# Kernel tuning notes

Measured on AMD Instinct MI355X. Metric: run time of the kernel, lower is better.

## Reference

```python
import jax, jax.numpy as jnp
import numpy as np

D_MODEL = 1024
NUM_HEAD = 16
HEAD_DIM = D_MODEL // NUM_HEAD
S, B = 2048, 2


def setup_inputs() -> dict:
    key = jax.random.key(0)
    ks = jax.random.split(key, 8)
    q = jax.random.normal(ks[0], (S, B, D_MODEL), dtype=jnp.float32)
    k = jax.random.normal(ks[1], (S, B, D_MODEL), dtype=jnp.float32)
    v = jax.random.normal(ks[2], (S, B, D_MODEL), dtype=jnp.float32)
    attn_mask = jnp.zeros((S, S), dtype=jnp.float32)
    # xavier_uniform_ bound for square (D,D) linear: sqrt(6/(D+D))
    bound = float(np.sqrt(6.0 / (D_MODEL + D_MODEL)))
    def w(k_):
        return jax.random.uniform(k_, (D_MODEL, D_MODEL), jnp.float32, -bound, bound)
    Wq, Wk, Wv, Wo = w(ks[3]), w(ks[4]), w(ks[5]), w(ks[6])
    zb = jnp.zeros((D_MODEL,), jnp.float32)
    return {"q": q, "k": k, "v": v, "attn_mask": attn_mask,
            "Wq": Wq, "bq": zb, "Wk": Wk, "bk": zb,
            "Wv": Wv, "bv": zb, "Wo": Wo, "bo": zb}


def reference(q, k, v, attn_mask, Wq, bq, Wk, bk, Wv, bv, Wo, bo):
    s, b, d = q.shape
    h, hd = NUM_HEAD, HEAD_DIM
    # QKV projections (torch Linear: x @ W.T + b)
    qp = q @ Wq.T + bq  # (S,B,D)
    kp = k @ Wk.T + bk
    vp = v @ Wv.T + bv
    # (S,B,H,Dh) -> permute(2,1,0,3) -> (H,B,S,Dh)
    qh = jnp.transpose(qp.reshape(s, b, h, hd), (2, 1, 0, 3))
    kh = jnp.transpose(kp.reshape(s, b, h, hd), (2, 1, 0, 3))
    vh = jnp.transpose(vp.reshape(s, b, h, hd), (2, 1, 0, 3))
    scores = jnp.einsum('hbqd,hbkd->hbqk', qh, kh) / jnp.sqrt(jnp.float32(hd))
    scores = scores + attn_mask  # additive mask broadcast over (H,B,*,*)
    weights = jax.nn.softmax(scores, axis=-1)
    out = jnp.einsum('hbqk,hbkd->hbqd', weights, vh)  # (H,B,S,Dh)
    # Faithful to original: raw contiguous view (H,B,S,Dh) -> (S,B,D)
    out = out.reshape(s, b, d)
    return out @ Wo.T + bo
```

## Files before the change

kernel.cpp:

```cpp
#include <hip/hip_runtime.h>
#include <hip/hip_bf16.h>
#include <cstdint>
#include <cstddef>

typedef unsigned short u16;
typedef short bf16x8 __attribute__((ext_vector_type(8)));
typedef short bf16x4 __attribute__((ext_vector_type(4)));
typedef unsigned short u16x8 __attribute__((ext_vector_type(8)));
typedef unsigned short u16x4 __attribute__((ext_vector_type(4)));
typedef float f32x4 __attribute__((ext_vector_type(4)));

#define S_LEN 2048
#define BATCH 2
#define DM 1024
#define NHEAD 16
#define HDIM 64
#define MROWS (S_LEN * BATCH)
#define LOG2E 1.44269504088896340736f
#define KSPLIT 2
#define SPAN (S_LEN / KSPLIT)
#define NROWS (NHEAD * BATCH * S_LEN)

__device__ __forceinline__ u16 f32_to_bf16(float f) {
  union { float f; uint32_t u; } v; v.f = f;
  uint32_t u = v.u;
  u += 0x7FFFu + ((u >> 16) & 1u);
  return (u16)(u >> 16);
}
__device__ __forceinline__ u16 cvt_bf16(float f) {
  __hip_bfloat16 h = __float2bfloat16(f);
  return *reinterpret_cast<u16*>(&h);
}
__device__ __forceinline__ float bf2f(u16 x) {
  union { float f; uint32_t u; } v; v.u = ((uint32_t)x) << 16; return v.f;
}

__device__ __forceinline__ void gload_lds16(const void* g, void* l) {
  __builtin_amdgcn_global_load_lds(
      (const __attribute__((address_space(1))) void*)g,
      (__attribute__((address_space(3))) void*)l, 16, 0, 0);
}

__device__ __forceinline__ bf16x4 tr_read(const void* lp) {
  bf16x4 d;
  auto p = (const __attribute__((address_space(3))) short*)lp;
  asm volatile("ds_read_b64_tr_b16 %0, %1" : "=v"(d) : "v"(p));
  return d;
}

#if __has_builtin(__builtin_amdgcn_mfma_f32_16x16x16_bf16)
#define MFMA16(a, b, c) __builtin_amdgcn_mfma_f32_16x16x16_bf16(a, b, c, 0, 0, 0)
#elif __has_builtin(__builtin_amdgcn_mfma_f32_16x16x16bf16_1k)
#define MFMA16(a, b, c) __builtin_amdgcn_mfma_f32_16x16x16bf16_1k(a, b, c, 0, 0, 0)
#else
__device__ __forceinline__ f32x4 mfma16_asm(bf16x4 a, bf16x4 b, f32x4 c) {
  f32x4 d;
  asm volatile("v_mfma_f32_16x16x16_bf16 %0, %1, %2, %3\n\ts_nop 7\n\ts_nop 7"
               : "=&v"(d) : "v"(a), "v"(b), "v"(c));
  return d;
}
#define MFMA16(a, b, c) mfma16_asm(a, b, c)
#endif

__global__ void cast4_f32_bf16(const float* __restrict__ s0, u16* __restrict__ d0,
                               const float* __restrict__ s1, u16* __restrict__ d1,
                               const float* __restrict__ s2, u16* __restrict__ d2,
                               const float* __restrict__ s3, u16* __restrict__ d3,
                               float4 scales, int n8) {
  const int which = blockIdx.y;
  const float* src = which == 0 ? s0 : which == 1 ? s1 : which == 2 ? s2 : s3;
  u16* dst = which == 0 ? d0 : which == 1 ? d1 : which == 2 ? d2 : d3;
  const float sc = which == 0 ? scales.x : which == 1 ? scales.y : which == 2 ? scales.z : scales.w;
  int i = blockIdx.x * blockDim.x + threadIdx.x;
  const int stride = gridDim.x * blockDim.x;
  for (; i < n8; i += stride) {
    const float4* s = (const float4*)(src + (size_t)i * 8);
    float4 a = s[0];
    float4 b = s[1];
    u16x8 o;
    o[0] = f32_to_bf16(a.x * sc); o[1] = f32_to_bf16(a.y * sc);
    o[2] = f32_to_bf16(a.z * sc); o[3] = f32_to_bf16(a.w * sc);
    o[4] = f32_to_bf16(b.x * sc); o[5] = f32_to_bf16(b.y * sc);
    o[6] = f32_to_bf16(b.z * sc); o[7] = f32_to_bf16(b.w * sc);
    *(u16x8*)(dst + (size_t)i * 8) = o;
  }
}

template <int MODE>
__global__ __launch_bounds__(256) void gemm_bt(
    const u16* __restrict__ A, const u16* __restrict__ Bw, const float* __restrict__ bias,
    float* __restrict__ outF, u16* __restrict__ outP, int M, int N, int K, float oscale)
{
  __shared__ u16 As[128 * 32];
  __shared__ u16 Bs[64 * 32];
  const int tid = threadIdx.x;
  const int wave = tid >> 6, lane = tid & 63;
  const int l15 = lane & 15, l4 = lane >> 4;
  const int wr = wave >> 1, wc = wave & 1;
  const int rowBase = blockIdx.y * 128, colBase = blockIdx.x * 64;

  f32x4 acc[4][2];
#pragma unroll
  for (int m = 0; m < 4; ++m)
#pragma unroll
    for (int n = 0; n < 2; ++n) acc[m][n] = (f32x4){0.f, 0.f, 0.f, 0.f};

  for (int k0 = 0; k0 < K; k0 += 32) {
#pragma unroll
    for (int c = 0; c < 2; ++c) {
      const int ldsbyte = wave * 2048 + c * 1024;
      const int elt = (ldsbyte >> 1) + lane * 8;
      const int r = elt >> 5, cc = elt & 31;
      gload_lds16(A + (size_t)(rowBase + r) * K + k0 + cc, (char*)As + ldsbyte);
    }
    {
      const int ldsbyte = wave * 1024;
      const int elt = (ldsbyte >> 1) + lane * 8;
      const int r = elt >> 5, cc = elt & 31;
      gload_lds16(Bw + (size_t)(colBase + r) * K + k0 + cc, (char*)Bs + ldsbyte);
    }
    __syncthreads();

    bf16x8 af[4], bfr[2];
#pragma unroll
    for (int m = 0; m < 4; ++m)
      af[m] = *(const bf16x8*)&As[(wr * 64 + m * 16 + l15) * 32 + 8 * l4];
#pragma unroll
    for (int n = 0; n < 2; ++n)
      bfr[n] = *(const bf16x8*)&Bs[(wc * 32 + n * 16 + l15) * 32 + 8 * l4];
#pragma unroll
    for (int m = 0; m < 4; ++m)
#pragma unroll
      for (int n = 0; n < 2; ++n)
        acc[m][n] = __builtin_amdgcn_mfma_f32_16x16x32_bf16(af[m], bfr[n], acc[m][n], 0, 0, 0);
    __syncthreads();
  }

#pragma unroll
  for (int m = 0; m < 4; ++m)
#pragma unroll
    for (int n = 0; n < 2; ++n)
#pragma unroll
      for (int j = 0; j < 4; ++j) {
        const int row = rowBase + wr * 64 + m * 16 + 4 * l4 + j;
        const int col = colBase + wc * 32 + n * 16 + l15;
        const float vv = (acc[m][n][j] + bias[col]) * oscale;
        if (MODE == 0) {
          const int s = row >> 1, b = row & 1, h = col >> 6, dh = col & 63;
          outP[((size_t)(h * BATCH + b) * S_LEN + s) * HDIM + dh] = f32_to_bf16(vv);
        } else {
          outF[(size_t)row * N + col] = vv;
        }
      }
}

__device__ __forceinline__ void stageK_swz(const u16* __restrict__ Kp, int kt, u16* dst, int tid) {
#pragma unroll
  for (int h = 0; h < 2; ++h) {
    const int c = tid + 256 * h;
    const int r = c >> 3, x = c & 7;
    gload_lds16(Kp + (size_t)(kt + r) * HDIM + (x ^ (r & 7)) * 8, (char*)dst + 16 * c);
  }
}
__device__ __forceinline__ void stageV(const u16* __restrict__ Vp, int kt, u16* dst, int tid) {
#pragma unroll
  for (int h = 0; h < 2; ++h) {
    const int c = tid + 256 * h;
    const int key = 4 * ((c >> 3) & 15) + ((c >> 1) & 3);
    const int dh  = 16 * (c >> 7) + 8 * (c & 1);
    gload_lds16(Vp + (size_t)(kt + key) * HDIM + dh, (char*)dst + 16 * c);
  }
}

__global__ __launch_bounds__(256, 4) void flash_attn(
    const u16* __restrict__ Qh, const u16* __restrict__ Kh, const u16* __restrict__ Vh,
    const u16* __restrict__ maskb, u16* __restrict__ Opart, float2* __restrict__ mlp)
{
  const int hb = blockIdx.y;
  const int z  = blockIdx.z;
  const int qb = blockIdx.x * 128;
  const int kbase = z * SPAN;
  const u16* Qp = Qh + (size_t)hb * S_LEN * HDIM;
  const u16* Kp = Kh + (size_t)hb * S_LEN * HDIM + (size_t)kbase * HDIM;
  const u16* Vp = Vh + (size_t)hb * S_LEN * HDIM + (size_t)kbase * HDIM;
  const u16* mp = maskb + kbase;
  const int tid = threadIdx.x;
  const int wave = tid >> 6, lane = tid & 63;
  const int l15 = lane & 15, l4 = lane >> 4;
  const int qrow0 = qb + wave * 32 + l15;
  const int qrow1 = qrow0 + 16;

  __shared__ u16 Klds[2][4096];
  __shared__ u16 Vlds[2][4096];

  bf16x8 bq[2][2];
  bq[0][0] = *(const bf16x8*)&Qp[(size_t)qrow0 * HDIM + 8 * l4];
  bq[0][1] = *(const bf16x8*)&Qp[(size_t)qrow0 * HDIM + 32 + 8 * l4];
  bq[1][0] = *(const bf16x8*)&Qp[(size_t)qrow1 * HDIM + 8 * l4];
  bq[1][1] = *(const bf16x8*)&Qp[(size_t)qrow1 * HDIM + 32 + 8 * l4];

  stageK_swz(Kp, 0, &Klds[0][0], tid);
  stageV(Vp, 0, &Vlds[0][0], tid);

  float m_run[2] = {-1e30f, -1e30f}, l_run[2] = {0.f, 0.f};
  f32x4 oacc[2][4];
#pragma unroll
  for (int f = 0; f < 2; ++f)
#pragma unroll
    for (int D = 0; D < 4; ++D) oacc[f][D] = (f32x4){0.f, 0.f, 0.f, 0.f};

  __syncthreads();

  for (int kt = 0; kt < SPAN; kt += 64) {
    const int cur = (kt >> 6) & 1;
    if (kt + 64 < SPAN) {
      stageK_swz(Kp, kt + 64, &Klds[cur ^ 1][0], tid);
      stageV(Vp, kt + 64, &Vlds[cur ^ 1][0], tid);
    }
    u16x4 mc[2][4];
#pragma unroll
    for (int kb = 0; kb < 4; ++kb) {
      mc[0][kb] = *(const u16x4*)&mp[(size_t)qrow0 * S_LEN + kt + 16 * kb + 4 * l4];
      mc[1][kb] = *(const u16x4*)&mp[(size_t)qrow1 * S_LEN + kt + 16 * kb + 4 * l4];
    }

    bf16x4 pb[2][4];
#pragma unroll
    for (int f = 0; f < 2; ++f) {
      f32x4 st[4];
#pragma unroll
      for (int kb = 0; kb < 4; ++kb) {
        const int r = 16 * kb + l15;
        const int s0 = (l4 ^ (l15 & 7)) * 8;
        const int s1 = ((l4 + 4) ^ (l15 & 7)) * 8;
        bf16x8 k0 = *(const bf16x8*)&Klds[cur][r * 64 + s0];
        bf16x8 k1 = *(const bf16x8*)&Klds[cur][r * 64 + s1];
        f32x4 zz = (f32x4){0.f, 0.f, 0.f, 0.f};
        zz = __builtin_amdgcn_mfma_f32_16x16x32_bf16(k0, bq[f][0], zz, 0, 0, 0);
        zz = __builtin_amdgcn_mfma_f32_16x16x32_bf16(k1, bq[f][1], zz, 0, 0, 0);
        st[kb] = zz;
      }
      float p[16];
#pragma unroll
      for (int kb = 0; kb < 4; ++kb)
#pragma unroll
        for (int j = 0; j < 4; ++j)
          p[4 * kb + j] = st[kb][j] + bf2f((u16)mc[f][kb][j]);

      float t0 = fmaxf(fmaxf(p[0], p[1]), fmaxf(p[2], p[3]));
      float t1 = fmaxf(fmaxf(p[4], p[5]), fmaxf(p[6], p[7]));
      float t2 = fmaxf(fmaxf(p[8], p[9]), fmaxf(p[10], p[11]));
      float t3 = fmaxf(fmaxf(p[12], p[13]), fmaxf(p[14], p[15]));
      float tm = fmaxf(fmaxf(t0, t1), fmaxf(t2, t3));
      tm = fmaxf(tm, __shfl_xor(tm, 16));
      tm = fmaxf(tm, __shfl_xor(tm, 32));

      if (!__all(tm - m_run[f] <= 11.0f)) {
        const float mn_ = fmaxf(m_run[f], tm);
        const float fac = exp2f(m_run[f] - mn_);
#pragma unroll
        for (int D = 0; D < 4; ++D)
#pragma unroll
          for (int j = 0; j < 4; ++j) oacc[f][D][j] *= fac;
        l_run[f] *= fac;
        m_run[f] = mn_;
      }

      float rs = 0.f;
#pragma unroll
      for (int kb = 0; kb < 4; ++kb)
#pragma unroll
        for (int e = 0; e < 4; ++e) {
          const float pe = exp2f(p[4 * kb + e] - m_run[f]);
          rs += pe;
          pb[f][kb][e] = (short)cvt_bf16(pe);
        }
      rs += __shfl_xor(rs, 16);
      rs += __shfl_xor(rs, 32);
      l_run[f] += rs;
    }

    const char* vb = (const char*)&Vlds[cur][0] + 8 * lane;
#pragma unroll
    for (int g = 0; g < 2; ++g) {
      bf16x4 va[2][4];
#pragma unroll
      for (int D = 0; D < 2; ++D)
#pragma unroll
        for (int kb = 0; kb < 4; ++kb)
          va[D][kb] = tr_read(vb + 2048 * (2 * g + D) + 512 * kb);
      asm volatile("s_waitcnt lgkmcnt(0)" ::: "memory");
      __builtin_amdgcn_sched_barrier(0);
#pragma unroll
      for (int D = 0; D < 2; ++D)
#pragma unroll
        for (int kb = 0; kb < 4; ++kb) {
          oacc[0][2 * g + D] = MFMA16(va[D][kb], pb[0][kb], oacc[0][2 * g + D]);
          oacc[1][2 * g + D] = MFMA16(va[D][kb], pb[1][kb], oacc[1][2 * g + D]);
        }
    }

    __syncthreads();
  }

  u16* Oz = Opart + (size_t)z * NROWS * HDIM;
#pragma unroll
  for (int f = 0; f < 2; ++f) {
    const float inv = 1.0f / l_run[f];
    const int qr = f == 0 ? qrow0 : qrow1;
    const size_t row = (size_t)hb * S_LEN + qr;
#pragma unroll
    for (int D = 0; D < 4; ++D) {
      u16x4 ov;
#pragma unroll
      for (int j = 0; j < 4; ++j) ov[j] = f32_to_bf16(oacc[f][D][j] * inv);
      *(u16x4*)&Oz[row * HDIM + 16 * D + 4 * l4] = ov;
    }
    if (l4 == 0) mlp[(size_t)z * NROWS + row] = make_float2(m_run[f], l_run[f]);
  }
}

__global__ __launch_bounds__(256) void fa_combine(
    const u16* __restrict__ Opart, const float2* __restrict__ mlp, u16* __restrict__ Ob)
{
  const int idx = blockIdx.x * blockDim.x + threadIdx.x;
  const int row = idx >> 4, c = idx & 15;
  const float2 a = mlp[row];
  const float2 b = mlp[NROWS + row];
  const float m = fmaxf(a.x, b.x);
  float w0 = exp2f(a.x - m) * a.y;
  float w1 = exp2f(b.x - m) * b.y;
  const float inv = 1.f / (w0 + w1);
  w0 *= inv; w1 *= inv;
  const size_t off = (size_t)row * HDIM + 4 * c;
  const u16x4 o0 = *(const u16x4*)&Opart[off];
  const u16x4 o1 = *(const u16x4*)&Opart[(size_t)NROWS * HDIM + off];
  u16x4 o;
#pragma unroll
  for (int j = 0; j < 4; ++j)
    o[j] = f32_to_bf16(w0 * bf2f((u16)o0[j]) + w1 * bf2f((u16)o1[j]));
  *(u16x4*)&Ob[off] = o;
}

extern "C" void kernel_launch(void* const* d_in, const int* in_sizes, int n_in,
                              void* d_out, int out_size, void* d_ws, size_t ws_size,
                              hipStream_t stream) {
  const float* q    = (const float*)d_in[0];
  const float* k    = (const float*)d_in[1];
  const float* v    = (const float*)d_in[2];
  const float* mask = (const float*)d_in[3];
  const float* Wq   = (const float*)d_in[4];
  const float* bq   = (const float*)d_in[5];
  const float* Wk   = (const float*)d_in[6];
  const float* bk   = (const float*)d_in[7];
  const float* Wv   = (const float*)d_in[8];
  const float* bv   = (const float*)d_in[9];
  const float* Wo   = (const float*)d_in[10];
  const float* bo   = (const float*)d_in[11];
  float* out = (float*)d_out;

  char* ws = (char*)d_ws;
  const size_t TEN = (size_t)MROWS * DM * sizeof(u16);
  const size_t WSZ = (size_t)DM * DM * sizeof(u16);
  u16* qb_ = (u16*)(ws);
  u16* kb_ = (u16*)(ws + TEN);
  u16* vb_ = (u16*)(ws + 2 * TEN);
  u16* wqb = (u16*)(ws + 3 * TEN);
  u16* wkb = (u16*)(ws + 3 * TEN + WSZ);
  u16* wvb = (u16*)(ws + 3 * TEN + 2 * WSZ);
  u16* wob = (u16*)(ws + 3 * TEN + 3 * WSZ);
  u16* Qh  = (u16*)(ws + 3 * TEN + 4 * WSZ);
  u16* Kh  = (u16*)(ws + 4 * TEN + 4 * WSZ);
  u16* Vh  = (u16*)(ws + 5 * TEN + 4 * WSZ);
  u16* Ob  = (u16*)(ws + 6 * TEN + 4 * WSZ);
  u16* maskb = (u16*)(ws + 7 * TEN + 4 * WSZ);
  u16* Opart = (u16*)(ws + 8 * TEN + 4 * WSZ);
  float2* mlp = (float2*)(ws + 10 * TEN + 4 * WSZ);

  const int n8_t = MROWS * DM / 8;
  const int n8_w = DM * DM / 8;
  cast4_f32_bf16<<<dim3(1024, 4), 256, 0, stream>>>(
      q, qb_, k, kb_, v, vb_, mask, maskb,
      make_float4(1.f, 1.f, 1.f, LOG2E), n8_t);
  cast4_f32_bf16<<<dim3(256, 4), 256, 0, stream>>>(
      Wq, wqb, Wk, wkb, Wv, wvb, Wo, wob,
      make_float4(1.f, 1.f, 1.f, 1.f), n8_w);

  const dim3 ggrid(DM / 64, MROWS / 128);
  const float qscale = 0.125f * LOG2E;
  gemm_bt<0><<<ggrid, 256, 0, stream>>>(qb_, wqb, bq, nullptr, Qh, MROWS, DM, DM, qscale);
  gemm_bt<0><<<ggrid, 256, 0, stream>>>(kb_, wkb, bk, nullptr, Kh, MROWS, DM, DM, 1.f);
  gemm_bt<0><<<ggrid, 256, 0, stream>>>(vb_, wvb, bv, nullptr, Vh, MROWS, DM, DM, 1.f);

  flash_attn<<<dim3(S_LEN / 128, NHEAD * BATCH, KSPLIT), 256, 0, stream>>>(
      Qh, Kh, Vh, maskb, Opart, mlp);
  fa_combine<<<NROWS * 16 / 256, 256, 0, stream>>>(Opart, mlp, Ob);

  gemm_bt<1><<<ggrid, 256, 0, stream>>>(Ob, wob, bo, out, nullptr, MROWS, DM, DM, 1.f);
}
```

Baseline: 204.7 us.

## Raise attention key split to four, batch QKV GEMMs, keep mask in fp32

The key-dimension split of flash attention goes from 2 to 4 so more workgroups run concurrently, and the combine kernel now merges an arbitrary number of partials. The three QKV projection GEMMs are launched as one grid with a z dimension to cut launch count and improve occupancy. The mask is scaled into an fp32 buffer by a separate kernel instead of being cast to bf16, which doubles mask read traffic inside attention. The workspace is repacked with aliasing (Opart overlaps the cast inputs), which saves memory but relies on those buffers being dead by then.

```diff
diff --git a/kernel.cpp b/kernel.cpp
--- a/kernel.cpp
+++ b/kernel.cpp
@@ -17,7 +17,7 @@
 #define HDIM 64
 #define MROWS (S_LEN * BATCH)
 #define LOG2E 1.44269504088896340736f
-#define KSPLIT 2
+#define KSPLIT 4
 #define SPAN (S_LEN / KSPLIT)
 #define NROWS (NHEAD * BATCH * S_LEN)
 
@@ -66,11 +66,10 @@
                                const float* __restrict__ s1, u16* __restrict__ d1,
                                const float* __restrict__ s2, u16* __restrict__ d2,
                                const float* __restrict__ s3, u16* __restrict__ d3,
-                               float4 scales, int n8) {
+                               int n8) {
   const int which = blockIdx.y;
   const float* src = which == 0 ? s0 : which == 1 ? s1 : which == 2 ? s2 : s3;
   u16* dst = which == 0 ? d0 : which == 1 ? d1 : which == 2 ? d2 : d3;
-  const float sc = which == 0 ? scales.x : which == 1 ? scales.y : which == 2 ? scales.z : scales.w;
   int i = blockIdx.x * blockDim.x + threadIdx.x;
   const int stride = gridDim.x * blockDim.x;
   for (; i < n8; i += stride) {
@@ -78,21 +77,32 @@
     float4 a = s[0];
     float4 b = s[1];
     u16x8 o;
-    o[0] = f32_to_bf16(a.x * sc); o[1] = f32_to_bf16(a.y * sc);
-    o[2] = f32_to_bf16(a.z * sc); o[3] = f32_to_bf16(a.w * sc);
-    o[4] = f32_to_bf16(b.x * sc); o[5] = f32_to_bf16(b.y * sc);
-    o[6] = f32_to_bf16(b.z * sc); o[7] = f32_to_bf16(b.w * sc);
+    o[0] = f32_to_bf16(a.x); o[1] = f32_to_bf16(a.y);
+    o[2] = f32_to_bf16(a.z); o[3] = f32_to_bf16(a.w);
+    o[4] = f32_to_bf16(b.x); o[5] = f32_to_bf16(b.y);
+    o[6] = f32_to_bf16(b.z); o[7] = f32_to_bf16(b.w);
     *(u16x8*)(dst + (size_t)i * 8) = o;
   }
 }
 
+__global__ void scale_f32(const float* __restrict__ src, float* __restrict__ dst,
+                          float sc, int n4) {
+  int i = blockIdx.x * blockDim.x + threadIdx.x;
+  const int stride = gridDim.x * blockDim.x;
+  for (; i < n4; i += stride) {
+    float4 a = *(const float4*)(src + (size_t)i * 4);
+    a.x *= sc; a.y *= sc; a.z *= sc; a.w *= sc;
+    *(float4*)(dst + (size_t)i * 4) = a;
+  }
+}
+
 template <int MODE>
-__global__ __launch_bounds__(256) void gemm_bt(
+__device__ __forceinline__ void gemm_body(
     const u16* __restrict__ A, const u16* __restrict__ Bw, const float* __restrict__ bias,
-    float* __restrict__ outF, u16* __restrict__ outP, int M, int N, int K, float oscale)
+    float* __restrict__ outF, u16* __restrict__ outP, float oscale,
+    u16* As, u16* Bs)
 {
-  __shared__ u16 As[128 * 32];
-  __shared__ u16 Bs[64 * 32];
+  const int K = DM, N = DM;
   const int tid = threadIdx.x;
   const int wave = tid >> 6, lane = tid & 63;
   const int l15 = lane & 15, l4 = lane >> 4;
@@ -154,6 +164,32 @@
       }
 }
 
+__global__ __launch_bounds__(256) void gemm_qkv(
+    const u16* __restrict__ Aq, const u16* __restrict__ Ak, const u16* __restrict__ Av,
+    const u16* __restrict__ Wq, const u16* __restrict__ Wk, const u16* __restrict__ Wv,
+    const float* __restrict__ bq, const float* __restrict__ bk, const float* __restrict__ bv,
+    u16* __restrict__ Oq, u16* __restrict__ Ok, u16* __restrict__ Ov, float qscale)
+{
+  __shared__ u16 As[128 * 32];
+  __shared__ u16 Bs[64 * 32];
+  const int z = blockIdx.z;
+  const u16* A  = z == 0 ? Aq : z == 1 ? Ak : Av;
+  const u16* W  = z == 0 ? Wq : z == 1 ? Wk : Wv;
+  const float* b = z == 0 ? bq : z == 1 ? bk : bv;
+  u16* O = z == 0 ? Oq : z == 1 ? Ok : Ov;
+  const float sc = z == 0 ? qscale : 1.f;
+  gemm_body<0>(A, W, b, nullptr, O, sc, As, Bs);
+}
+
+__global__ __launch_bounds__(256) void gemm_out(
+    const u16* __restrict__ A, const u16* __restrict__ W, const float* __restrict__ bias,
+    float* __restrict__ outF)
+{
+  __shared__ u16 As[128 * 32];
+  __shared__ u16 Bs[64 * 32];
+  gemm_body<1>(A, W, bias, outF, nullptr, 1.f, As, Bs);
+}
+
 __device__ __forceinline__ void stageK_swz(const u16* __restrict__ Kp, int kt, u16* dst, int tid) {
 #pragma unroll
   for (int h = 0; h < 2; ++h) {
@@ -174,7 +210,7 @@
 
 __global__ __launch_bounds__(256, 4) void flash_attn(
     const u16* __restrict__ Qh, const u16* __restrict__ Kh, const u16* __restrict__ Vh,
-    const u16* __restrict__ maskb, u16* __restrict__ Opart, float2* __restrict__ mlp)
+    const float* __restrict__ maskf, u16* __restrict__ Opart, float2* __restrict__ mlp)
 {
   const int hb = blockIdx.y;
   const int z  = blockIdx.z;
@@ -183,7 +219,7 @@
   const u16* Qp = Qh + (size_t)hb * S_LEN * HDIM;
   const u16* Kp = Kh + (size_t)hb * S_LEN * HDIM + (size_t)kbase * HDIM;
   const u16* Vp = Vh + (size_t)hb * S_LEN * HDIM + (size_t)kbase * HDIM;
-  const u16* mp = maskb + kbase;
+  const float* mp = maskf + kbase;
   const int tid = threadIdx.x;
   const int wave = tid >> 6, lane = tid & 63;
   const int l15 = lane & 15, l4 = lane >> 4;
@@ -217,11 +253,11 @@
       stageK_swz(Kp, kt + 64, &Klds[cur ^ 1][0], tid);
       stageV(Vp, kt + 64, &Vlds[cur ^ 1][0], tid);
     }
-    u16x4 mc[2][4];
+    float4 mc[2][4];
 #pragma unroll
     for (int kb = 0; kb < 4; ++kb) {
-      mc[0][kb] = *(const u16x4*)&mp[(size_t)qrow0 * S_LEN + kt + 16 * kb + 4 * l4];
-      mc[1][kb] = *(const u16x4*)&mp[(size_t)qrow1 * S_LEN + kt + 16 * kb + 4 * l4];
+      mc[0][kb] = *(const float4*)&mp[(size_t)qrow0 * S_LEN + kt + 16 * kb + 4 * l4];
+      mc[1][kb] = *(const float4*)&mp[(size_t)qrow1 * S_LEN + kt + 16 * kb + 4 * l4];
     }
 
     bf16x4 pb[2][4];
@@ -242,10 +278,12 @@
       }
       float p[16];
 #pragma unroll
-      for (int kb = 0; kb < 4; ++kb)
-#pragma unroll
-        for (int j = 0; j < 4; ++j)
-          p[4 * kb + j] = st[kb][j] + bf2f((u16)mc[f][kb][j]);
+      for (int kb = 0; kb < 4; ++kb) {
+        p[4 * kb + 0] = st[kb][0] + mc[f][kb].x;
+        p[4 * kb + 1] = st[kb][1] + mc[f][kb].y;
+        p[4 * kb + 2] = st[kb][2] + mc[f][kb].z;
+        p[4 * kb + 3] = st[kb][3] + mc[f][kb].w;
+      }
 
       float t0 = fmaxf(fmaxf(p[0], p[1]), fmaxf(p[2], p[3]));
       float t1 = fmaxf(fmaxf(p[4], p[5]), fmaxf(p[6], p[7]));
@@ -325,20 +363,34 @@
 {
   const int idx = blockIdx.x * blockDim.x + threadIdx.x;
   const int row = idx >> 4, c = idx & 15;
-  const float2 a = mlp[row];
-  const float2 b = mlp[NROWS + row];
-  const float m = fmaxf(a.x, b.x);
-  float w0 = exp2f(a.x - m) * a.y;
-  float w1 = exp2f(b.x - m) * b.y;
-  const float inv = 1.f / (w0 + w1);
-  w0 *= inv; w1 *= inv;
+  float2 ml[KSPLIT];
+  float m = -1e30f;
+#pragma unroll
+  for (int zz = 0; zz < KSPLIT; ++zz) {
+    ml[zz] = mlp[(size_t)zz * NROWS + row];
+    m = fmaxf(m, ml[zz].x);
+  }
+  float w[KSPLIT], tot = 0.f;
+#pragma unroll
+  for (int zz = 0; zz < KSPLIT; ++zz) {
+    w[zz] = exp2f(ml[zz].x - m) * ml[zz].y;
+    tot += w[zz];
+  }
+  const float inv = 1.f / tot;
   const size_t off = (size_t)row * HDIM + 4 * c;
-  const u16x4 o0 = *(const u16x4*)&Opart[off];
-  const u16x4 o1 = *(const u16x4*)&Opart[(size_t)NROWS * HDIM + off];
+  float a0 = 0.f, a1 = 0.f, a2 = 0.f, a3 = 0.f;
+#pragma unroll
+  for (int zz = 0; zz < KSPLIT; ++zz) {
+    const u16x4 o = *(const u16x4*)&Opart[(size_t)zz * NROWS * HDIM + off];
+    const float wz = w[zz] * inv;
+    a0 += wz * bf2f((u16)o[0]);
+    a1 += wz * bf2f((u16)o[1]);
+    a2 += wz * bf2f((u16)o[2]);
+    a3 += wz * bf2f((u16)o[3]);
+  }
   u16x4 o;
-#pragma unroll
-  for (int j = 0; j < 4; ++j)
-    o[j] = f32_to_bf16(w0 * bf2f((u16)o0[j]) + w1 * bf2f((u16)o1[j]));
+  o[0] = f32_to_bf16(a0); o[1] = f32_to_bf16(a1);
+  o[2] = f32_to_bf16(a2); o[3] = f32_to_bf16(a3);
   *(u16x4*)&Ob[off] = o;
 }
 
@@ -360,41 +412,37 @@
   float* out = (float*)d_out;
 
   char* ws = (char*)d_ws;
-  const size_t TEN = (size_t)MROWS * DM * sizeof(u16);
-  const size_t WSZ = (size_t)DM * DM * sizeof(u16);
-  u16* qb_ = (u16*)(ws);
-  u16* kb_ = (u16*)(ws + TEN);
-  u16* vb_ = (u16*)(ws + 2 * TEN);
-  u16* wqb = (u16*)(ws + 3 * TEN);
-  u16* wkb = (u16*)(ws + 3 * TEN + WSZ);
-  u16* wvb = (u16*)(ws + 3 * TEN + 2 * WSZ);
-  u16* wob = (u16*)(ws + 3 * TEN + 3 * WSZ);
-  u16* Qh  = (u16*)(ws + 3 * TEN + 4 * WSZ);
-  u16* Kh  = (u16*)(ws + 4 * TEN + 4 * WSZ);
-  u16* Vh  = (u16*)(ws + 5 * TEN + 4 * WSZ);
-  u16* Ob  = (u16*)(ws + 6 * TEN + 4 * WSZ);
-  u16* maskb = (u16*)(ws + 7 * TEN + 4 * WSZ);
-  u16* Opart = (u16*)(ws + 8 * TEN + 4 * WSZ);
-  float2* mlp = (float2*)(ws + 10 * TEN + 4 * WSZ);
+  const size_t MB = 1024 * 1024;
+  u16*  Qh    = (u16*)(ws + 0 * MB);
+  u16*  Kh    = (u16*)(ws + 8 * MB);
+  u16*  Vh    = (u16*)(ws + 16 * MB);
+  float* maskf = (float*)(ws + 24 * MB);
+  u16*  wob   = (u16*)(ws + 40 * MB);
+  u16*  Ob    = (u16*)(ws + 42 * MB);
+  u16*  qb_   = (u16*)(ws + 50 * MB);
+  u16*  kb_   = (u16*)(ws + 58 * MB);
+  u16*  vb_   = (u16*)(ws + 66 * MB);
+  u16*  wqb   = (u16*)(ws + 74 * MB);
+  u16*  wkb   = (u16*)(ws + 76 * MB);
+  u16*  wvb   = (u16*)(ws + 78 * MB);
+  u16*  Opart = (u16*)(ws + 50 * MB);
+  float2* mlp = (float2*)(ws + 82 * MB);
 
   const int n8_t = MROWS * DM / 8;
   const int n8_w = DM * DM / 8;
-  cast4_f32_bf16<<<dim3(1024, 4), 256, 0, stream>>>(
-      q, qb_, k, kb_, v, vb_, mask, maskb,
-      make_float4(1.f, 1.f, 1.f, LOG2E), n8_t);
+  cast4_f32_bf16<<<dim3(1024, 3), 256, 0, stream>>>(
+      q, qb_, k, kb_, v, vb_, q, qb_, n8_t);
   cast4_f32_bf16<<<dim3(256, 4), 256, 0, stream>>>(
-      Wq, wqb, Wk, wkb, Wv, wvb, Wo, wob,
-      make_float4(1.f, 1.f, 1.f, 1.f), n8_w);
-
-  const dim3 ggrid(DM / 64, MROWS / 128);
+      Wq, wqb, Wk, wkb, Wv, wvb, Wo, wob, n8_w);
+  scale_f32<<<2048, 256, 0, stream>>>(mask, maskf, LOG2E, S_LEN * S_LEN / 4);
+
   const float qscale = 0.125f * LOG2E;
-  gemm_bt<0><<<ggrid, 256, 0, stream>>>(qb_, wqb, bq, nullptr, Qh, MROWS, DM, DM, qscale);
-  gemm_bt<0><<<ggrid, 256, 0, stream>>>(kb_, wkb, bk, nullptr, Kh, MROWS, DM, DM, 1.f);
-  gemm_bt<0><<<ggrid, 256, 0, stream>>>(vb_, wvb, bv, nullptr, Vh, MROWS, DM, DM, 1.f);
+  gemm_qkv<<<dim3(DM / 64, MROWS / 128, 3), 256, 0, stream>>>(
+      qb_, kb_, vb_, wqb, wkb, wvb, bq, bk, bv, Qh, Kh, Vh, qscale);
 
   flash_attn<<<dim3(S_LEN / 128, NHEAD * BATCH, KSPLIT), 256, 0, stream>>>(
-      Qh, Kh, Vh, maskb, Opart, mlp);
+      Qh, Kh, Vh, maskf, Opart, mlp);
   fa_combine<<<NROWS * 16 / 256, 256, 0, stream>>>(Opart, mlp, Ob);
 
-  gemm_bt<1><<<ggrid, 256, 0, stream>>>(Ob, wob, bo, out, nullptr, MROWS, DM, DM, 1.f);
-}
+  gemm_out<<<dim3(DM / 64, MROWS / 128), 256, 0, stream>>>(Ob, wob, bo, out);
+}
```

New measurement: 220.1 us. 7.5% more time.
